# Kernel tuning notes

Measured on AMD Instinct MI355X. Metric: run time of the kernel, lower is better.

The kernel has to match this reference:

```python
import jax, jax.numpy as jnp
import numpy as np

B, S, D = 2, 2048, 1024
H = 16
HD = D // H


def setup_inputs() -> dict:
    key = jax.random.key(0)
    ks = jax.random.split(key, 6)
    x = jax.random.normal(ks[0], (B, S, D), dtype=jnp.float32)
    scale = 1.0 / np.sqrt(D)
    Wq = jax.random.normal(ks[1], (D, D), dtype=jnp.float32) * scale
    Wk = jax.random.normal(ks[2], (D, D), dtype=jnp.float32) * scale
    Wv = jax.random.normal(ks[3], (D, D), dtype=jnp.float32) * scale
    Wo = jax.random.normal(ks[4], (D, D), dtype=jnp.float32) * scale
    bo = jax.random.normal(ks[5], (D,), dtype=jnp.float32) * 0.01
    return {"x": x, "Wq": Wq, "Wk": Wk, "Wv": Wv, "Wo": Wo, "bo": bo}


def reference(x, Wq, Wk, Wv, Wo, bo):
    b, t, _ = x.shape
    # QKV projections (no bias), split into heads: [b, h, t, hd]
    q = (x @ Wq).reshape(b, t, H, HD).transpose(0, 2, 1, 3)
    k = (x @ Wk).reshape(b, t, H, HD).transpose(0, 2, 1, 3)
    v = (x @ Wv).reshape(b, t, H, HD).transpose(0, 2, 1, 3)
    # scores [b, h, t, t]; causal mask (upper triangle -> -inf) applied before scaling
    scores = jnp.einsum("bhqd,bhkd->bhqk", q, k)
    causal = jnp.triu(jnp.ones((t, t), dtype=bool), k=1)
    scores = jnp.where(causal, -jnp.inf, scores)
    attn = jax.nn.softmax(scores / jnp.sqrt(jnp.asarray(HD, scores.dtype)), axis=-1)
    ctx = jnp.einsum("bhqk,bhkd->bhqd", attn, v)
    ctx = ctx.transpose(0, 2, 1, 3).reshape(b, t, H * HD)
    return ctx @ Wo + bo
```

## Files before the change

kernel.cpp:

```cpp
#include <hip/hip_runtime.h>

#define B_ 2
#define S_ 2048
#define D_ 1024
#define H_ 16
#define HD_ 64
#define M_ (B_*S_)

typedef __attribute__((ext_vector_type(8))) short bf16x8;
typedef __attribute__((ext_vector_type(4))) short s16x4;
typedef __attribute__((ext_vector_type(4))) float f32x4;
typedef __attribute__((ext_vector_type(4))) unsigned int u32x4;

static __device__ __forceinline__ unsigned short f2bf(float f) {
  unsigned int u = __builtin_bit_cast(unsigned int, f);
  u += 0x7FFFu + ((u >> 16) & 1u);
  return (unsigned short)(u >> 16);
}

static __device__ __forceinline__ unsigned int cvt_pk_bf16(float a, float b) {
  unsigned int r;
  asm("v_cvt_pk_bf16_f32 %0, %1, %2" : "=v"(r) : "v"(a), "v"(b));
  return r;
}

static __device__ __forceinline__ void gload_lds16(const void* g, void* l) {
  __builtin_amdgcn_global_load_lds(
      (const __attribute__((address_space(1))) unsigned int*)g,
      (__attribute__((address_space(3))) unsigned int*)l, 16, 0, 0);
}

__global__ __launch_bounds__(256) void xcvt_kernel(const float* __restrict__ x,
                                                   unsigned short* __restrict__ xb) {
  size_t i = ((size_t)blockIdx.x * 256 + threadIdx.x) * 8;
  float4 a = ((const float4*)(x + i))[0];
  float4 b = ((const float4*)(x + i))[1];
  bf16x8 w;
  w[0]=(short)f2bf(a.x); w[1]=(short)f2bf(a.y); w[2]=(short)f2bf(a.z); w[3]=(short)f2bf(a.w);
  w[4]=(short)f2bf(b.x); w[5]=(short)f2bf(b.y); w[6]=(short)f2bf(b.z); w[7]=(short)f2bf(b.w);
  *(bf16x8*)(xb + i) = w;
}

__global__ void wtrans_kernel(const float* __restrict__ Wq, const float* __restrict__ Wk,
                              const float* __restrict__ Wv, const float* __restrict__ Wo,
                              unsigned short* __restrict__ wt) {
  __shared__ float tile[32][33];
  const float* W = blockIdx.z==0 ? Wq : blockIdx.z==1 ? Wk : blockIdx.z==2 ? Wv : Wo;
  unsigned short* out = wt + (size_t)blockIdx.z * D_ * D_;
  int n0 = blockIdx.x*32, k0 = blockIdx.y*32;
  int tx = threadIdx.x, ty = threadIdx.y;
  #pragma unroll
  for (int i=0;i<4;i++) tile[ty+i*8][tx] = W[(size_t)(k0+ty+i*8)*D_ + n0+tx];
  __syncthreads();
  #pragma unroll
  for (int i=0;i<4;i++) out[(size_t)(n0+ty+i*8)*D_ + (k0+tx)] = f2bf(tile[tx][ty+i*8]);
}

#define GEMM_K_LOOP(Abase, Bbase)                                                     \
  for (int ks = 0; ks < 16; ++ks) {                                                   \
    const int k0 = ks * 64;                                                           \
    __syncthreads();                                                                  \
    _Pragma("unroll")                                                                 \
    for (int p = 0; p < 4; ++p) {                                                     \
      int c = p*256 + t;                                                              \
      int row = c >> 3, sl = (c & 7) ^ (row & 7);                                     \
      gload_lds16(Abase + (size_t)row*D_ + k0 + sl*8, &As[(p*256 + wid*64)*8]);       \
    }                                                                                 \
    _Pragma("unroll")                                                                 \
    for (int p = 0; p < 4; ++p) {                                                     \
      int c = p*256 + t;                                                              \
      int row = c >> 3, sl = (c & 7) ^ (row & 7);                                     \
      gload_lds16(Bbase + (size_t)row*D_ + k0 + sl*8, &Bs[(p*256 + wid*64)*8]);       \
    }                                                                                 \
    __syncthreads();                                                                  \
    _Pragma("unroll")                                                                 \
    for (int kk = 0; kk < 2; ++kk) {                                                  \
      bf16x8 af[4], bfr[4];                                                           \
      _Pragma("unroll")                                                               \
      for (int m = 0; m < 4; ++m) {                                                   \
        int row = wr + m*16 + l15;                                                    \
        af[m] = *(const bf16x8*)((const char*)As + row*128 + (((kk*4+lg)^(row&7))<<4)); \
      }                                                                               \
      _Pragma("unroll")                                                               \
      for (int n = 0; n < 4; ++n) {                                                   \
        int row = wc + n*16 + l15;                                                    \
        bfr[n] = *(const bf16x8*)((const char*)Bs + row*128 + (((kk*4+lg)^(row&7))<<4)); \
      }                                                                               \
      _Pragma("unroll")                                                               \
      for (int m = 0; m < 4; ++m)                                                     \
        _Pragma("unroll")                                                             \
        for (int n = 0; n < 4; ++n)                                                   \
          acc[m][n] = __builtin_amdgcn_mfma_f32_16x16x32_bf16(af[m], bfr[n], acc[m][n], 0,0,0); \
    }                                                                                 \
  }

__global__ __launch_bounds__(256,3) void gemm_qkv_kernel(
    const unsigned short* __restrict__ xb, const unsigned short* __restrict__ wt,
    unsigned short* __restrict__ Qo, unsigned short* __restrict__ Ko,
    unsigned short* __restrict__ Vto) {
  __shared__ __align__(16) unsigned short As[128*64];
  __shared__ __align__(16) unsigned short Bs[128*64];
  const int z = blockIdx.z;
  const int m0 = blockIdx.y*128, n0 = blockIdx.x*128;
  const int t = threadIdx.x, lane = t & 63, wid = t >> 6;
  const int wr = (wid>>1)*64, wc = (wid&1)*64;
  const int l15 = lane & 15, lg = lane >> 4;
  const unsigned short* Ab = xb + (size_t)m0 * D_;
  const unsigned short* Bb = wt + (size_t)z * D_ * D_ + (size_t)n0 * D_;

  f32x4 acc[4][4];
  #pragma unroll
  for (int m=0;m<4;m++)
    #pragma unroll
    for (int n=0;n<4;n++) acc[m][n] = f32x4{0.f,0.f,0.f,0.f};

  GEMM_K_LOOP(Ab, Bb)

  #pragma unroll
  for (int m=0;m<4;m++) {
    #pragma unroll
    for (int n=0;n<4;n++) {
      #pragma unroll
      for (int r=0;r<4;r++) {
        int gm = m0 + wr + m*16 + lg*4 + r;
        int gn = n0 + wc + n*16 + l15;
        int b = gm >> 11, s = gm & (S_-1);
        int h = gn >> 6,  d = gn & 63;
        unsigned short val = f2bf(acc[m][n][r]);
        if (z==0)      Qo[(((size_t)(b*H_+h))*S_ + s)*HD_ + d] = val;
        else if (z==1) Ko[(((size_t)(b*H_+h))*S_ + s)*HD_ + d] = val;
        else           Vto[(((size_t)(b*H_+h))*HD_ + d)*S_ + s] = val;
      }
    }
  }
}

__global__ __launch_bounds__(256,3) void attn_kernel(
    const unsigned short* __restrict__ Q, const unsigned short* __restrict__ K,
    const unsigned short* __restrict__ Vt, unsigned short* __restrict__ ctx) {
  __shared__ __align__(16) unsigned short KT[2][64*64];
  __shared__ __align__(16) unsigned short VT[2][64*64];
  __shared__ __align__(16) unsigned short PL[4][16*72];
  const int t = threadIdx.x, lane = t & 63, wid = t >> 6;
  const int bh = blockIdx.x & 31;
  const int qt = 31 - (int)(blockIdx.x >> 5);
  const int b = bh >> 4, h = bh & 15;
  const int q0 = qt * 64, qw0 = q0 + wid * 16;
  const int nchunk = qt + 1;
  const unsigned short* Qp = Q  + (size_t)bh * S_ * HD_;
  const unsigned short* Kp = K  + (size_t)bh * S_ * HD_;
  const unsigned short* Vp = Vt + (size_t)bh * HD_ * S_;
  const int l15 = lane & 15, lg = lane >> 4;
  const int rsub = lane >> 3, slot = lane & 7;
  const int sslot = slot ^ rsub;

  bf16x8 qf0 = *(const bf16x8*)(Qp + (size_t)(qw0 + l15)*HD_ + lg*8);
  bf16x8 qf1 = *(const bf16x8*)(Qp + (size_t)(qw0 + l15)*HD_ + 32 + lg*8);

  f32x4 o[4];
  #pragma unroll
  for (int dt=0;dt<4;dt++) o[dt] = f32x4{0.f,0.f,0.f,0.f};
  float m = -INFINITY, lsum = 0.f;
  const float c = 0.18033688011112042f;
  const float THRS = 44.36141955583649f;

  auto stage = [&](int ch, int buf) {
    const int kk0 = ch * 64;
    #pragma unroll
    for (int j=0;j<2;j++) {
      int row = 16*wid + 8*j + rsub;
      gload_lds16(Kp + (size_t)(kk0 + row)*HD_ + sslot*8, &KT[buf][(16*wid + 8*j)*64]);
      gload_lds16(Vp + (size_t)row*S_ + kk0 + sslot*8,    &VT[buf][(16*wid + 8*j)*64]);
    }
  };

  stage(0, 0);
  __syncthreads();

  for (int ch=0; ch<nchunk; ++ch) {
    const int cur = ch & 1;
    const int kk0 = ch * 64;
    if (ch + 1 < nchunk) stage(ch+1, cur^1);

    const unsigned short* Kt = &KT[cur][0];
    const unsigned short* Vv = &VT[cur][0];

    f32x4 st[4];
    #pragma unroll
    for (int kt=0; kt<4; ++kt) {
      int row = kt*16 + l15;
      int sw = (row & 7) << 4;
      bf16x8 kf0 = *(const bf16x8*)((const char*)Kt + row*128 + ((lg*16)      ^ sw));
      bf16x8 kf1 = *(const bf16x8*)((const char*)Kt + row*128 + ((64 + lg*16) ^ sw));
      f32x4 z = f32x4{0.f,0.f,0.f,0.f};
      z = __builtin_amdgcn_mfma_f32_16x16x32_bf16(kf0, qf0, z, 0,0,0);
      z = __builtin_amdgcn_mfma_f32_16x16x32_bf16(kf1, qf1, z, 0,0,0);
      st[kt] = z;
    }

    if (ch == nchunk-1) {
      const int q = qw0 + l15;
      #pragma unroll
      for (int kt=0;kt<4;kt++)
        #pragma unroll
        for (int r=0;r<4;r++)
          if (kk0 + kt*16 + lg*4 + r > q) st[kt][r] = -INFINITY;
    }

    float mx = st[0][0];
    #pragma unroll
    for (int kt=0;kt<4;kt++)
      #pragma unroll
      for (int r=0;r<4;r++) mx = fmaxf(mx, st[kt][r]);
    mx = fmaxf(mx, __shfl_xor(mx, 16));
    mx = fmaxf(mx, __shfl_xor(mx, 32));

    if (__any(mx > m + THRS)) {
      float mn = fmaxf(m, mx);
      float corr = exp2f((m - mn) * c);
      m = mn;
      lsum *= corr;
      float oc[4];
      #pragma unroll
      for (int r=0;r<4;r++) oc[r] = __shfl(corr, lg*4 + r);
      #pragma unroll
      for (int dt=0;dt<4;dt++)
        #pragma unroll
        for (int r=0;r<4;r++) o[dt][r] *= oc[r];
    }

    float rs = 0.f;
    #pragma unroll
    for (int kt=0;kt<4;kt++) {
      #pragma unroll
      for (int r=0;r<4;r++) {
        float p = exp2f((st[kt][r] - m) * c);
        st[kt][r] = p;
        rs += p;
      }
      uint2 pk;
      pk.x = cvt_pk_bf16(st[kt][0], st[kt][1]);
      pk.y = cvt_pk_bf16(st[kt][2], st[kt][3]);
      *(uint2*)&PL[wid][l15*72 + kt*16 + lg*4] = pk;
    }
    rs += __shfl_xor(rs, 16);
    rs += __shfl_xor(rs, 32);
    lsum += rs;

    bf16x8 pf0 = *(const bf16x8*)&PL[wid][l15*72 + lg*8];
    bf16x8 pf1 = *(const bf16x8*)&PL[wid][l15*72 + 32 + lg*8];

    #pragma unroll
    for (int dt=0;dt<4;dt++) {
      int row = dt*16 + l15;
      int sw = (row & 7) << 4;
      bf16x8 vf0 = *(const bf16x8*)((const char*)Vv + row*128 + ((lg*16)      ^ sw));
      bf16x8 vf1 = *(const bf16x8*)((const char*)Vv + row*128 + ((64 + lg*16) ^ sw));
      o[dt] = __builtin_amdgcn_mfma_f32_16x16x32_bf16(pf0, vf0, o[dt], 0,0,0);
      o[dt] = __builtin_amdgcn_mfma_f32_16x16x32_bf16(pf1, vf1, o[dt], 0,0,0);
    }

    __syncthreads();
  }

  float li = 1.f / lsum;
  float lr[4];
  #pragma unroll
  for (int r=0;r<4;r++) lr[r] = __shfl(li, lg*4 + r);
  #pragma unroll
  for (int dt=0;dt<4;dt++)
    #pragma unroll
    for (int r=0;r<4;r++) {
      size_t row = (size_t)(b*S_ + qw0 + lg*4 + r);
      ctx[row*D_ + h*HD_ + dt*16 + l15] = f2bf(o[dt][r] * lr[r]);
    }
}

__global__ __launch_bounds__(256,3) void gemm_out_kernel(
    const unsigned short* __restrict__ ctx, const unsigned short* __restrict__ WtO,
    const float* __restrict__ bo, float* __restrict__ out) {
  __shared__ __align__(16) unsigned short As[128*64];
  __shared__ __align__(16) unsigned short Bs[128*64];
  const int m0 = blockIdx.y*128, n0 = blockIdx.x*128;
  const int t = threadIdx.x, lane = t & 63, wid = t >> 6;
  const int wr = (wid>>1)*64, wc = (wid&1)*64;
  const int l15 = lane & 15, lg = lane >> 4;
  const unsigned short* Ab = ctx + (size_t)m0 * D_;
  const unsigned short* Bb = WtO + (size_t)n0 * D_;

  f32x4 acc[4][4];
  #pragma unroll
  for (int m=0;m<4;m++)
    #pragma unroll
    for (int n=0;n<4;n++) acc[m][n] = f32x4{0.f,0.f,0.f,0.f};

  GEMM_K_LOOP(Ab, Bb)

  #pragma unroll
  for (int n=0;n<4;n++) {
    float bias = bo[n0 + wc + n*16 + l15];
    #pragma unroll
    for (int m=0;m<4;m++)
      #pragma unroll
      for (int r=0;r<4;r++) {
        int gm = m0 + wr + m*16 + lg*4 + r;
        int gn = n0 + wc + n*16 + l15;
        out[(size_t)gm*D_ + gn] = acc[m][n][r] + bias;
      }
  }
}

extern "C" void kernel_launch(void* const* d_in, const int* in_sizes, int n_in,
                              void* d_out, int out_size, void* d_ws, size_t ws_size,
                              hipStream_t stream) {
  (void)in_sizes; (void)n_in; (void)out_size; (void)ws_size;
  const float* x  = (const float*)d_in[0];
  const float* Wq = (const float*)d_in[1];
  const float* Wk = (const float*)d_in[2];
  const float* Wv = (const float*)d_in[3];
  const float* Wo = (const float*)d_in[4];
  const float* bo = (const float*)d_in[5];
  float* out = (float*)d_out;

  unsigned short* wt  = (unsigned short*)d_ws;
  unsigned short* Qb  = wt  + (size_t)4*D_*D_;
  unsigned short* Kb  = Qb  + (size_t)M_*D_;
  unsigned short* Vtb = Kb  + (size_t)M_*D_;
  unsigned short* ctb = Vtb + (size_t)M_*D_;
  unsigned short* xbb = ctb + (size_t)M_*D_;

  xcvt_kernel<<<dim3(M_*D_/(256*8)), 256, 0, stream>>>(x, xbb);
  wtrans_kernel<<<dim3(32,32,4), dim3(32,8), 0, stream>>>(Wq, Wk, Wv, Wo, wt);
  gemm_qkv_kernel<<<dim3(8,32,3), 256, 0, stream>>>(xbb, wt, Qb, Kb, Vtb);
  attn_kernel<<<dim3(1024), 256, 0, stream>>>(Qb, Kb, Vtb, ctb);
  gemm_out_kernel<<<dim3(8,32), 256, 0, stream>>>(ctb, wt + (size_t)3*D_*D_, bo, out);
}
```

Measured before the change: 119.8 us.

## Process 128 query rows per attention block with two 16-row tiles per wave

Each attention block now handles 128 queries (32 per wave, split into two 16-row sub-tiles), so every K/V chunk staged in LDS is reused by twice as many queries and the grid halves to 512 blocks. Waves skip chunks that lie entirely above their causal diagonal, and masking is applied only to chunks crossing the diagonal. The P staging buffer is reorganised with an XOR swizzle instead of padding. In exchange the kernel uses more registers and LDS, which may lower occupancy, and there are fewer blocks to balance across CUs.

```diff
diff --git a/kernel.cpp b/kernel.cpp
--- a/kernel.cpp
+++ b/kernel.cpp
@@ -140,27 +140,30 @@
     const unsigned short* __restrict__ Vt, unsigned short* __restrict__ ctx) {
   __shared__ __align__(16) unsigned short KT[2][64*64];
   __shared__ __align__(16) unsigned short VT[2][64*64];
-  __shared__ __align__(16) unsigned short PL[4][16*72];
+  __shared__ __align__(16) unsigned short PL[4][2][16*64];
   const int t = threadIdx.x, lane = t & 63, wid = t >> 6;
   const int bh = blockIdx.x & 31;
-  const int qt = 31 - (int)(blockIdx.x >> 5);
+  const int qb = 15 - (int)(blockIdx.x >> 5);
   const int b = bh >> 4, h = bh & 15;
-  const int q0 = qt * 64, qw0 = q0 + wid * 16;
-  const int nchunk = qt + 1;
+  const int q0 = qb * 128, qw0 = q0 + wid * 32;
+  const int nchunk = 2*qb + 2;
   const unsigned short* Qp = Q  + (size_t)bh * S_ * HD_;
   const unsigned short* Kp = K  + (size_t)bh * S_ * HD_;
   const unsigned short* Vp = Vt + (size_t)bh * HD_ * S_;
   const int l15 = lane & 15, lg = lane >> 4;
   const int rsub = lane >> 3, slot = lane & 7;
   const int sslot = slot ^ rsub;
-
-  bf16x8 qf0 = *(const bf16x8*)(Qp + (size_t)(qw0 + l15)*HD_ + lg*8);
-  bf16x8 qf1 = *(const bf16x8*)(Qp + (size_t)(qw0 + l15)*HD_ + 32 + lg*8);
-
-  f32x4 o[4];
-  #pragma unroll
-  for (int dt=0;dt<4;dt++) o[dt] = f32x4{0.f,0.f,0.f,0.f};
-  float m = -INFINITY, lsum = 0.f;
+  const int swp = (l15 & 7) << 4;
+
+  bf16x8 qfA0 = *(const bf16x8*)(Qp + (size_t)(qw0 + l15)*HD_ + lg*8);
+  bf16x8 qfA1 = *(const bf16x8*)(Qp + (size_t)(qw0 + l15)*HD_ + 32 + lg*8);
+  bf16x8 qfB0 = *(const bf16x8*)(Qp + (size_t)(qw0 + 16 + l15)*HD_ + lg*8);
+  bf16x8 qfB1 = *(const bf16x8*)(Qp + (size_t)(qw0 + 16 + l15)*HD_ + 32 + lg*8);
+
+  f32x4 oA[4], oB[4];
+  #pragma unroll
+  for (int dt=0;dt<4;dt++) { oA[dt] = f32x4{0.f,0.f,0.f,0.f}; oB[dt] = f32x4{0.f,0.f,0.f,0.f}; }
+  float mA = -INFINITY, mB = -INFINITY, lA = 0.f, lB = 0.f;
   const float c = 0.18033688011112042f;
   const float THRS = 44.36141955583649f;
 
@@ -182,98 +185,116 @@
     const int kk0 = ch * 64;
     if (ch + 1 < nchunk) stage(ch+1, cur^1);
 
-    const unsigned short* Kt = &KT[cur][0];
-    const unsigned short* Vv = &VT[cur][0];
-
-    f32x4 st[4];
-    #pragma unroll
-    for (int kt=0; kt<4; ++kt) {
-      int row = kt*16 + l15;
-      int sw = (row & 7) << 4;
-      bf16x8 kf0 = *(const bf16x8*)((const char*)Kt + row*128 + ((lg*16)      ^ sw));
-      bf16x8 kf1 = *(const bf16x8*)((const char*)Kt + row*128 + ((64 + lg*16) ^ sw));
-      f32x4 z = f32x4{0.f,0.f,0.f,0.f};
-      z = __builtin_amdgcn_mfma_f32_16x16x32_bf16(kf0, qf0, z, 0,0,0);
-      z = __builtin_amdgcn_mfma_f32_16x16x32_bf16(kf1, qf1, z, 0,0,0);
-      st[kt] = z;
+    if (kk0 <= qw0 + 31) {
+      const unsigned short* Kt = &KT[cur][0];
+      const unsigned short* Vv = &VT[cur][0];
+
+      f32x4 stA[4], stB[4];
+      #pragma unroll
+      for (int kt=0; kt<4; ++kt) {
+        int row = kt*16 + l15;
+        int sw2 = (row & 7) << 4;
+        bf16x8 kf0 = *(const bf16x8*)((const char*)Kt + row*128 + ((lg*16)      ^ sw2));
+        bf16x8 kf1 = *(const bf16x8*)((const char*)Kt + row*128 + ((64 + lg*16) ^ sw2));
+        f32x4 zA = f32x4{0.f,0.f,0.f,0.f}, zB = f32x4{0.f,0.f,0.f,0.f};
+        zA = __builtin_amdgcn_mfma_f32_16x16x32_bf16(kf0, qfA0, zA, 0,0,0);
+        zA = __builtin_amdgcn_mfma_f32_16x16x32_bf16(kf1, qfA1, zA, 0,0,0);
+        zB = __builtin_amdgcn_mfma_f32_16x16x32_bf16(kf0, qfB0, zB, 0,0,0);
+        zB = __builtin_amdgcn_mfma_f32_16x16x32_bf16(kf1, qfB1, zB, 0,0,0);
+        stA[kt] = zA; stB[kt] = zB;
+      }
+
+      if (kk0 + 63 > qw0) {
+        const int qA = qw0 + l15, qB = qA + 16;
+        #pragma unroll
+        for (int kt=0;kt<4;kt++)
+          #pragma unroll
+          for (int r=0;r<4;r++) {
+            int kidx = kk0 + kt*16 + lg*4 + r;
+            if (kidx > qA) stA[kt][r] = -INFINITY;
+            if (kidx > qB) stB[kt][r] = -INFINITY;
+          }
+      }
+
+      float mxA = fmaxf(fmaxf(stA[0][0], stA[0][1]), fmaxf(stA[0][2], stA[0][3]));
+      float mxB = fmaxf(fmaxf(stB[0][0], stB[0][1]), fmaxf(stB[0][2], stB[0][3]));
+      #pragma unroll
+      for (int kt=1;kt<4;kt++) {
+        mxA = fmaxf(mxA, fmaxf(fmaxf(stA[kt][0], stA[kt][1]), fmaxf(stA[kt][2], stA[kt][3])));
+        mxB = fmaxf(mxB, fmaxf(fmaxf(stB[kt][0], stB[kt][1]), fmaxf(stB[kt][2], stB[kt][3])));
+      }
+      mxA = fmaxf(mxA, __shfl_xor(mxA, 16)); mxA = fmaxf(mxA, __shfl_xor(mxA, 32));
+      mxB = fmaxf(mxB, __shfl_xor(mxB, 16)); mxB = fmaxf(mxB, __shfl_xor(mxB, 32));
+
+      if (__any((mxA > mA + THRS) || (mxB > mB + THRS))) {
+        float mnA = fmaxf(mA, mxA), mnB = fmaxf(mB, mxB);
+        float corrA = exp2f((mA - mnA) * c), corrB = exp2f((mB - mnB) * c);
+        mA = mnA; mB = mnB;
+        lA *= corrA; lB *= corrB;
+        #pragma unroll
+        for (int r=0;r<4;r++) {
+          float ocA = __shfl(corrA, lg*4 + r), ocB = __shfl(corrB, lg*4 + r);
+          #pragma unroll
+          for (int dt=0;dt<4;dt++) { oA[dt][r] *= ocA; oB[dt][r] *= ocB; }
+        }
+      }
+
+      float rsA = 0.f, rsB = 0.f;
+      #pragma unroll
+      for (int kt=0;kt<4;kt++) {
+        #pragma unroll
+        for (int r=0;r<4;r++) {
+          float pA = exp2f((stA[kt][r] - mA) * c);
+          float pB = exp2f((stB[kt][r] - mB) * c);
+          stA[kt][r] = pA; stB[kt][r] = pB;
+          rsA += pA; rsB += pB;
+        }
+        uint2 pkA, pkB;
+        pkA.x = cvt_pk_bf16(stA[kt][0], stA[kt][1]);
+        pkA.y = cvt_pk_bf16(stA[kt][2], stA[kt][3]);
+        pkB.x = cvt_pk_bf16(stB[kt][0], stB[kt][1]);
+        pkB.y = cvt_pk_bf16(stB[kt][2], stB[kt][3]);
+        int off = l15*128 + ((kt*32 + lg*8) ^ swp);
+        *(uint2*)((char*)&PL[wid][0][0] + off) = pkA;
+        *(uint2*)((char*)&PL[wid][1][0] + off) = pkB;
+      }
+      rsA += __shfl_xor(rsA, 16); rsA += __shfl_xor(rsA, 32);
+      rsB += __shfl_xor(rsB, 16); rsB += __shfl_xor(rsB, 32);
+      lA += rsA; lB += rsB;
+
+      bf16x8 pfA0 = *(const bf16x8*)((const char*)&PL[wid][0][0] + l15*128 + ((lg*16)      ^ swp));
+      bf16x8 pfA1 = *(const bf16x8*)((const char*)&PL[wid][0][0] + l15*128 + ((64 + lg*16) ^ swp));
+      bf16x8 pfB0 = *(const bf16x8*)((const char*)&PL[wid][1][0] + l15*128 + ((lg*16)      ^ swp));
+      bf16x8 pfB1 = *(const bf16x8*)((const char*)&PL[wid][1][0] + l15*128 + ((64 + lg*16) ^ swp));
+
+      #pragma unroll
+      for (int dt=0;dt<4;dt++) {
+        int row = dt*16 + l15;
+        int sw2 = (row & 7) << 4;
+        bf16x8 vf0 = *(const bf16x8*)((const char*)Vv + row*128 + ((lg*16)      ^ sw2));
+        bf16x8 vf1 = *(const bf16x8*)((const char*)Vv + row*128 + ((64 + lg*16) ^ sw2));
+        oA[dt] = __builtin_amdgcn_mfma_f32_16x16x32_bf16(pfA0, vf0, oA[dt], 0,0,0);
+        oA[dt] = __builtin_amdgcn_mfma_f32_16x16x32_bf16(pfA1, vf1, oA[dt], 0,0,0);
+        oB[dt] = __builtin_amdgcn_mfma_f32_16x16x32_bf16(pfB0, vf0, oB[dt], 0,0,0);
+        oB[dt] = __builtin_amdgcn_mfma_f32_16x16x32_bf16(pfB1, vf1, oB[dt], 0,0,0);
+      }
     }
 
-    if (ch == nchunk-1) {
-      const int q = qw0 + l15;
-      #pragma unroll
-      for (int kt=0;kt<4;kt++)
-        #pragma unroll
-        for (int r=0;r<4;r++)
-          if (kk0 + kt*16 + lg*4 + r > q) st[kt][r] = -INFINITY;
+    __syncthreads();
+  }
+
+  float liA = 1.f / lA, liB = 1.f / lB;
+  #pragma unroll
+  for (int r=0;r<4;r++) {
+    float lrA = __shfl(liA, lg*4 + r), lrB = __shfl(liB, lg*4 + r);
+    size_t rowA = (size_t)(b*S_ + qw0 + lg*4 + r);
+    size_t rowB = rowA + 16;
+    #pragma unroll
+    for (int dt=0;dt<4;dt++) {
+      ctx[rowA*D_ + h*HD_ + dt*16 + l15] = f2bf(oA[dt][r] * lrA);
+      ctx[rowB*D_ + h*HD_ + dt*16 + l15] = f2bf(oB[dt][r] * lrB);
     }
-
-    float mx = st[0][0];
-    #pragma unroll
-    for (int kt=0;kt<4;kt++)
-      #pragma unroll
-      for (int r=0;r<4;r++) mx = fmaxf(mx, st[kt][r]);
-    mx = fmaxf(mx, __shfl_xor(mx, 16));
-    mx = fmaxf(mx, __shfl_xor(mx, 32));
-
-    if (__any(mx > m + THRS)) {
-      float mn = fmaxf(m, mx);
-      float corr = exp2f((m - mn) * c);
-      m = mn;
-      lsum *= corr;
-      float oc[4];
-      #pragma unroll
-      for (int r=0;r<4;r++) oc[r] = __shfl(corr, lg*4 + r);
-      #pragma unroll
-      for (int dt=0;dt<4;dt++)
-        #pragma unroll
-        for (int r=0;r<4;r++) o[dt][r] *= oc[r];
-    }
-
-    float rs = 0.f;
-    #pragma unroll
-    for (int kt=0;kt<4;kt++) {
-      #pragma unroll
-      for (int r=0;r<4;r++) {
-        float p = exp2f((st[kt][r] - m) * c);
-        st[kt][r] = p;
-        rs += p;
-      }
-      uint2 pk;
-      pk.x = cvt_pk_bf16(st[kt][0], st[kt][1]);
-      pk.y = cvt_pk_bf16(st[kt][2], st[kt][3]);
-      *(uint2*)&PL[wid][l15*72 + kt*16 + lg*4] = pk;
-    }
-    rs += __shfl_xor(rs, 16);
-    rs += __shfl_xor(rs, 32);
-    lsum += rs;
-
-    bf16x8 pf0 = *(const bf16x8*)&PL[wid][l15*72 + lg*8];
-    bf16x8 pf1 = *(const bf16x8*)&PL[wid][l15*72 + 32 + lg*8];
-
-    #pragma unroll
-    for (int dt=0;dt<4;dt++) {
-      int row = dt*16 + l15;
-      int sw = (row & 7) << 4;
-      bf16x8 vf0 = *(const bf16x8*)((const char*)Vv + row*128 + ((lg*16)      ^ sw));
-      bf16x8 vf1 = *(const bf16x8*)((const char*)Vv + row*128 + ((64 + lg*16) ^ sw));
-      o[dt] = __builtin_amdgcn_mfma_f32_16x16x32_bf16(pf0, vf0, o[dt], 0,0,0);
-      o[dt] = __builtin_amdgcn_mfma_f32_16x16x32_bf16(pf1, vf1, o[dt], 0,0,0);
-    }
-
-    __syncthreads();
-  }
-
-  float li = 1.f / lsum;
-  float lr[4];
-  #pragma unroll
-  for (int r=0;r<4;r++) lr[r] = __shfl(li, lg*4 + r);
-  #pragma unroll
-  for (int dt=0;dt<4;dt++)
-    #pragma unroll
-    for (int r=0;r<4;r++) {
-      size_t row = (size_t)(b*S_ + qw0 + lg*4 + r);
-      ctx[row*D_ + h*HD_ + dt*16 + l15] = f2bf(o[dt][r] * lr[r]);
-    }
+  }
 }
 
 __global__ __launch_bounds__(256,3) void gemm_out_kernel(
@@ -332,6 +353,6 @@
   xcvt_kernel<<<dim3(M_*D_/(256*8)), 256, 0, stream>>>(x, xbb);
   wtrans_kernel<<<dim3(32,32,4), dim3(32,8), 0, stream>>>(Wq, Wk, Wv, Wo, wt);
   gemm_qkv_kernel<<<dim3(8,32,3), 256, 0, stream>>>(xbb, wt, Qb, Kb, Vtb);
-  attn_kernel<<<dim3(1024), 256, 0, stream>>>(Qb, Kb, Vtb, ctb);
+  attn_kernel<<<dim3(512), 256, 0, stream>>>(Qb, Kb, Vtb, ctb);
   gemm_out_kernel<<<dim3(8,32), 256, 0, stream>>>(ctb, wt + (size_t)3*D_*D_, bo, out);
 }
```

New measurement: 135.1 us. 1.13x slower.
